# Performance work log

Hardware: AMD Instinct MI355X
Metric: run time of the kernel (lower is better)

## Reference

```python
import jax, jax.numpy as jnp
import numpy as np

A, D, H, NACT = 8, 128, 64, 16  # n_agents, input_shape, rnn_hidden_dim, n_actions
B = 16384


def setup_inputs() -> dict:
    key = jax.random.key(0)
    ks = jax.random.split(key, 12)
    s = 1.0 / np.sqrt(H)
    si = 1.0 / np.sqrt(D)
    inp = {
        'inputs': jax.random.normal(ks[0], (B * A, D), dtype=jnp.float32),
        'hidden_state': jax.random.normal(ks[1], (B, A, H), dtype=jnp.float32),
        # stacked per-agent (non-shared) weights, PyTorch default-init scale
        'W1': jax.random.uniform(ks[2], (A, H, D), jnp.float32, -si, si),
        'b1': jax.random.uniform(ks[3], (A, H), jnp.float32, -si, si),
        'W_ih': jax.random.uniform(ks[4], (A, 3 * H, H), jnp.float32, -s, s),
        'b_ih': jax.random.uniform(ks[5], (A, 3 * H), jnp.float32, -s, s),
        'W_hh': jax.random.uniform(ks[6], (A, 3 * H, H), jnp.float32, -s, s),
        'b_hh': jax.random.uniform(ks[7], (A, 3 * H), jnp.float32, -s, s),
        'W2': jax.random.uniform(ks[8], (A, NACT, H), jnp.float32, -s, s),
        'b2': jax.random.uniform(ks[9], (A, NACT), jnp.float32, -s, s),
    }
    return inp


def reference(inputs, hidden_state, W1, b1, W_ih, b_ih, W_hh, b_hh, W2, b2):
    x = inputs.reshape(-1, A, D)                 # [B, A, D]
    h = hidden_state.reshape(-1, A, H)           # [B, A, H]
    # fc1 + ReLU, batched over agents
    z1 = jax.nn.relu(jnp.einsum('bad,ahd->bah', x, W1) + b1)
    # GRUCell (PyTorch convention: gates r, z, n)
    gi = jnp.einsum('bah,agh->bag', z1, W_ih) + b_ih   # [B, A, 3H]
    gh = jnp.einsum('bah,agh->bag', h, W_hh) + b_hh
    i_r, i_z, i_n = jnp.split(gi, 3, axis=-1)
    h_r, h_z, h_n = jnp.split(gh, 3, axis=-1)
    r = jax.nn.sigmoid(i_r + h_r)
    z = jax.nn.sigmoid(i_z + h_z)
    n = jnp.tanh(i_n + r * h_n)
    h_new = (1.0 - z) * n + z * h                # [B, A, H]
    # fc2
    q = jnp.einsum('bah,anh->ban', h_new, W2) + b2   # [B, A, NACT]
    # match torch: cat(qs, dim=-1).view(-1, n_actions) == reshape [B*A, NACT]
    return q.reshape(-1, NACT), h_new
```

## Files before the change

kernel.cpp:

```cpp
#include <hip/hip_runtime.h>
#include <hip/hip_bf16.h>
#include <cstddef>

#define NAGENT 8
#define DIN    128
#define HID    64
#define NACT   16

typedef __attribute__((ext_vector_type(8))) short bf16x8;
typedef __attribute__((ext_vector_type(4))) float f32x4;

__device__ __forceinline__ short f2bf(float f) {
    __hip_bfloat16 h = __float2bfloat16(f);
    union { __hip_bfloat16 h; short s; } u; u.h = h;
    return u.s;
}
__device__ __forceinline__ float sigmoid_f(float v) { return 1.0f / (1.0f + __expf(-v)); }
__device__ __forceinline__ float tanh_f(float v) {
    v = fminf(fmaxf(v, -15.0f), 15.0f);
    float e = __expf(2.0f * v);
    return (e - 1.0f) / (e + 1.0f);
}
__device__ __forceinline__ bf16x8 cvt8pair(float4 v0, float4 v1) {
    bf16x8 r;
    r[0] = f2bf(v0.x); r[1] = f2bf(v0.y); r[2] = f2bf(v0.z); r[3] = f2bf(v0.w);
    r[4] = f2bf(v1.x); r[5] = f2bf(v1.y); r[6] = f2bf(v1.z); r[7] = f2bf(v1.w);
    return r;
}
__device__ __forceinline__ void gload_lds16(const void* g, void* l) {
    __builtin_amdgcn_global_load_lds(
        (const __attribute__((address_space(1))) unsigned int*)g,
        (__attribute__((address_space(3))) unsigned int*)l, 16, 0, 0);
}

extern "C" __global__ void __launch_bounds__(256)
conv_weights_packed(const float* __restrict__ W1, const float* __restrict__ Wih,
                    const float* __restrict__ Whh, const float* __restrict__ W2,
                    short* __restrict__ ws)
{
    const int a = blockIdx.y;
    const int c = blockIdx.x * 256 + threadIdx.x;
    if (c >= 4224) return;
    const int lane = c & 63, lr = lane & 15, lk = lane >> 4;
    const float* src;
    if (c < 1024) {
        int n = c >> 8, k = (c >> 6) & 3;
        src = W1 + a * 8192 + (n * 16 + lr) * 128 + k * 32 + lk * 8;
    } else if (c < 2560) {
        int idx = (c - 1024) >> 6;
        int g = idx >> 3, n = (idx >> 1) & 3, kk = idx & 1;
        src = Wih + a * 12288 + (g * 64 + n * 16 + lr) * 64 + kk * 32 + lk * 8;
    } else if (c < 4096) {
        int idx = (c - 2560) >> 6;
        int g = idx >> 3, n = (idx >> 1) & 3, kk = idx & 1;
        src = Whh + a * 12288 + (g * 64 + n * 16 + lr) * 64 + kk * 32 + lk * 8;
    } else {
        int kk = (c - 4096) >> 6;
        src = W2 + a * 1024 + lr * 64 + kk * 32 + lk * 8;
    }
    float4 v0 = ((const float4*)src)[0];
    float4 v1 = ((const float4*)src)[1];
    bf16x8 o = cvt8pair(v0, v1);
    *(bf16x8*)(ws + (size_t)a * 33792 + (size_t)c * 8) = o;
}

extern "C" __global__ void __launch_bounds__(256, 4)
rnn_main(const float* __restrict__ x,
         const float* __restrict__ hin,
         const float* __restrict__ b1, const float* __restrict__ bih,
         const float* __restrict__ bhh, const float* __restrict__ b2,
         const short* __restrict__ wsp,
         float* __restrict__ qout,
         float* __restrict__ hout)
{
    const int bid  = blockIdx.x;
    const int a    = bid & 7;
    const int t    = threadIdx.x;
    const int wid  = t >> 6;
    const int lane = t & 63;
    const int lr   = lane & 15;
    const int lk   = lane >> 4;

    __shared__ short wbuf[6144];
    __shared__ short zs[4 * 1024];
    char* zb = (char*)(zs + wid * 1024);

    const short* wsA = wsp + (size_t)a * 33792;
    const int tile = (bid >> 3) * 4 + wid;
    const int arow = tile * 16 + lr;

    const float* xrow = x + ((size_t)arow * NAGENT + a) * DIN + lk * 8;
    const float* hrow = hin + ((size_t)arow * NAGENT + a) * HID + lk * 8;

    gload_lds16(wsA + (size_t)(wid * 2 + 0) * 512 + lane * 8, wbuf + (wid * 2 + 0) * 512);
    gload_lds16(wsA + (size_t)(wid * 2 + 1) * 512 + lane * 8, wbuf + (wid * 2 + 1) * 512);

    bf16x8 xf[4];
    #pragma unroll
    for (int k = 0; k < 4; ++k)
        xf[k] = cvt8pair(*(const float4*)(xrow + k * 32),
                         *(const float4*)(xrow + k * 32 + 4));
    bf16x8 hf0 = cvt8pair(*(const float4*)(hrow),      *(const float4*)(hrow + 4));
    bf16x8 hf1 = cvt8pair(*(const float4*)(hrow + 32), *(const float4*)(hrow + 36));

    f32x4 acc1[4];
    #pragma unroll
    for (int n = 0; n < 4; ++n) {
        float bv = b1[a * HID + n * 16 + lr];
        acc1[n] = (f32x4){bv, bv, bv, bv};
    }

    __syncthreads();

    #pragma unroll
    for (int k = 0; k < 4; ++k)
        #pragma unroll
        for (int n = 0; n < 2; ++n) {
            bf16x8 wb = *(const bf16x8*)(wbuf + ((n * 4 + k) * 64 + lane) * 8);
            acc1[n] = __builtin_amdgcn_mfma_f32_16x16x32_bf16(xf[k], wb, acc1[n], 0, 0, 0);
        }
    __syncthreads();

    gload_lds16(wsA + (size_t)(8 + wid * 2 + 0) * 512 + lane * 8, wbuf + (wid * 2 + 0) * 512);
    gload_lds16(wsA + (size_t)(8 + wid * 2 + 1) * 512 + lane * 8, wbuf + (wid * 2 + 1) * 512);
    __syncthreads();

    #pragma unroll
    for (int k = 0; k < 4; ++k)
        #pragma unroll
        for (int n = 2; n < 4; ++n) {
            bf16x8 wb = *(const bf16x8*)(wbuf + (((n * 4 + k) - 8) * 64 + lane) * 8);
            acc1[n] = __builtin_amdgcn_mfma_f32_16x16x32_bf16(xf[k], wb, acc1[n], 0, 0, 0);
        }
    #pragma unroll
    for (int n = 0; n < 4; ++n)
        #pragma unroll
        for (int j = 0; j < 4; ++j) {
            int row = lk * 4 + j, col = n * 16 + lr;
            *(short*)(zb + row * 128 + ((col * 2) ^ ((row & 7) << 4))) =
                f2bf(fmaxf(acc1[n][j], 0.0f));
        }

    bf16x8 za0 = *(const bf16x8*)(zb + lr * 128 + ((0 * 64 + lk * 16) ^ ((lr & 7) << 4)));
    bf16x8 za1 = *(const bf16x8*)(zb + lr * 128 + ((1 * 64 + lk * 16) ^ ((lr & 7) << 4)));

    #pragma unroll 1
    for (int n = 0; n < 4; ++n) {
        __syncthreads();
        #pragma unroll
        for (int si = 0; si < 3; ++si) {
            int s = wid + si * 4;
            int round = (s < 6) ? (16 + ((s >> 1) * 4 + n) * 2 + (s & 1))
                                : (40 + (((s - 6) >> 1) * 4 + n) * 2 + ((s - 6) & 1));
            gload_lds16(wsA + (size_t)round * 512 + lane * 8, wbuf + s * 512);
        }
        float hp[4];
        #pragma unroll
        for (int j = 0; j < 4; ++j)
            hp[j] = hin[((size_t)(tile * 16 + lk * 4 + j) * NAGENT + a) * HID + n * 16 + lr];
        float bhr = bhh[a * 192 +   0 + n * 16 + lr];
        float bhz = bhh[a * 192 +  64 + n * 16 + lr];
        float bhn = bhh[a * 192 + 128 + n * 16 + lr];
        float bir = bih[a * 192 +   0 + n * 16 + lr];
        float biz = bih[a * 192 +  64 + n * 16 + lr];
        float bin_ = bih[a * 192 + 128 + n * 16 + lr];
        __syncthreads();

        f32x4 aHr = (f32x4){bhr, bhr, bhr, bhr};
        f32x4 aHz = (f32x4){bhz, bhz, bhz, bhz};
        f32x4 aHn = (f32x4){bhn, bhn, bhn, bhn};
        f32x4 aIr = (f32x4){bir, bir, bir, bir};
        f32x4 aIz = (f32x4){biz, biz, biz, biz};
        f32x4 aIn = (f32x4){bin_, bin_, bin_, bin_};
        #pragma unroll
        for (int kk = 0; kk < 2; ++kk) {
            bf16x8 hfk = kk ? hf1 : hf0;
            bf16x8 zak = kk ? za1 : za0;
            bf16x8 wir = *(const bf16x8*)(wbuf + ((0 * 2 + kk) * 64 + lane) * 8);
            bf16x8 wiz = *(const bf16x8*)(wbuf + ((1 * 2 + kk) * 64 + lane) * 8);
            bf16x8 win = *(const bf16x8*)(wbuf + ((2 * 2 + kk) * 64 + lane) * 8);
            bf16x8 whr = *(const bf16x8*)(wbuf + ((6 + 0 * 2 + kk) * 64 + lane) * 8);
            bf16x8 whz = *(const bf16x8*)(wbuf + ((6 + 1 * 2 + kk) * 64 + lane) * 8);
            bf16x8 whn = *(const bf16x8*)(wbuf + ((6 + 2 * 2 + kk) * 64 + lane) * 8);
            aHr = __builtin_amdgcn_mfma_f32_16x16x32_bf16(hfk, whr, aHr, 0, 0, 0);
            aHz = __builtin_amdgcn_mfma_f32_16x16x32_bf16(hfk, whz, aHz, 0, 0, 0);
            aHn = __builtin_amdgcn_mfma_f32_16x16x32_bf16(hfk, whn, aHn, 0, 0, 0);
            aIr = __builtin_amdgcn_mfma_f32_16x16x32_bf16(zak, wir, aIr, 0, 0, 0);
            aIz = __builtin_amdgcn_mfma_f32_16x16x32_bf16(zak, wiz, aIz, 0, 0, 0);
            aIn = __builtin_amdgcn_mfma_f32_16x16x32_bf16(zak, win, aIn, 0, 0, 0);
        }

        #pragma unroll
        for (int j = 0; j < 4; ++j) {
            int row = lk * 4 + j, col = n * 16 + lr;
            float r  = sigmoid_f(aIr[j] + aHr[j]);
            float zv = sigmoid_f(aIz[j] + aHz[j]);
            float nn = tanh_f(aIn[j] + r * aHn[j]);
            float hv = (1.0f - zv) * nn + zv * hp[j];
            hout[((size_t)(tile * 16 + row) * NAGENT + a) * HID + col] = hv;
            *(short*)(zb + row * 128 + ((col * 2) ^ ((row & 7) << 4))) = f2bf(hv);
        }
    }

    {
        float bq = b2[a * NACT + lr];
        f32x4 q = (f32x4){bq, bq, bq, bq};
        bf16x8 ha0 = *(const bf16x8*)(zb + lr * 128 + ((0 * 64 + lk * 16) ^ ((lr & 7) << 4)));
        bf16x8 ha1 = *(const bf16x8*)(zb + lr * 128 + ((1 * 64 + lk * 16) ^ ((lr & 7) << 4)));
        bf16x8 w2f0 = *(const bf16x8*)(wsA + 32768 + (0 * 64 + lane) * 8);
        bf16x8 w2f1 = *(const bf16x8*)(wsA + 32768 + (1 * 64 + lane) * 8);
        q = __builtin_amdgcn_mfma_f32_16x16x32_bf16(ha0, w2f0, q, 0, 0, 0);
        q = __builtin_amdgcn_mfma_f32_16x16x32_bf16(ha1, w2f1, q, 0, 0, 0);
        #pragma unroll
        for (int j = 0; j < 4; ++j)
            qout[((size_t)(tile * 16 + lk * 4 + j) * NAGENT + a) * NACT + lr] = q[j];
    }
}

extern "C" void kernel_launch(void* const* d_in, const int* in_sizes, int n_in,
                              void* d_out, int out_size, void* d_ws, size_t ws_size,
                              hipStream_t stream)
{
    const float* x   = (const float*)d_in[0];
    const float* hin = (const float*)d_in[1];
    const float* W1  = (const float*)d_in[2];
    const float* b1  = (const float*)d_in[3];
    const float* Wih = (const float*)d_in[4];
    const float* bih = (const float*)d_in[5];
    const float* Whh = (const float*)d_in[6];
    const float* bhh = (const float*)d_in[7];
    const float* W2  = (const float*)d_in[8];
    const float* b2  = (const float*)d_in[9];

    const int B = in_sizes[0] / (NAGENT * DIN);

    float* qout = (float*)d_out;
    float* hout = (float*)d_out + (size_t)B * NAGENT * NACT;

    short* wsp = (short*)d_ws;

    conv_weights_packed<<<dim3(17, NAGENT), 256, 0, stream>>>(W1, Wih, Whh, W2, wsp);

    dim3 grid((B / 64) * NAGENT);
    rnn_main<<<grid, 256, 0, stream>>>(x, hin, b1, bih, bhh, b2, wsp, qout, hout);
}
```

Baseline: 48.71 us.

## Double-buffer weight staging in LDS to overlap loads with MFMA

```diff
diff --git a/kernel.cpp b/kernel.cpp
--- a/kernel.cpp
+++ b/kernel.cpp
@@ -81,20 +81,26 @@
     const int lr   = lane & 15;
     const int lk   = lane >> 4;
 
-    __shared__ short wbuf[6144];
+    __shared__ short wbuf[2 * 3072];
     __shared__ short zs[4 * 1024];
     char* zb = (char*)(zs + wid * 1024);
+    const char* wb0 = (const char*)wbuf;
+    const char* wb1 = (const char*)(wbuf + 3072);
 
     const short* wsA = wsp + (size_t)a * 33792;
     const int tile = (bid >> 3) * 4 + wid;
     const int arow = tile * 16 + lr;
 
+    #define STAGE6(dstbuf, REXPR)                                                   \
+        { int s = wid;  int rr = (REXPR);                                           \
+          gload_lds16(wsA + (size_t)rr * 512 + lane * 8, (dstbuf) + s * 512);       \
+          if (wid < 2) { s = wid + 4; rr = (REXPR);                                 \
+            gload_lds16(wsA + (size_t)rr * 512 + lane * 8, (dstbuf) + s * 512); } }
+
+    STAGE6(wbuf, s)
+
     const float* xrow = x + ((size_t)arow * NAGENT + a) * DIN + lk * 8;
     const float* hrow = hin + ((size_t)arow * NAGENT + a) * HID + lk * 8;
-
-    gload_lds16(wsA + (size_t)(wid * 2 + 0) * 512 + lane * 8, wbuf + (wid * 2 + 0) * 512);
-    gload_lds16(wsA + (size_t)(wid * 2 + 1) * 512 + lane * 8, wbuf + (wid * 2 + 1) * 512);
-
     bf16x8 xf[4];
     #pragma unroll
     for (int k = 0; k < 4; ++k)
@@ -102,104 +108,110 @@
                          *(const float4*)(xrow + k * 32 + 4));
     bf16x8 hf0 = cvt8pair(*(const float4*)(hrow),      *(const float4*)(hrow + 4));
     bf16x8 hf1 = cvt8pair(*(const float4*)(hrow + 32), *(const float4*)(hrow + 36));
+    float b1v[4];
+    #pragma unroll
+    for (int n = 0; n < 4; ++n) b1v[n] = b1[a * HID + n * 16 + lr];
 
     f32x4 acc1[4];
     #pragma unroll
-    for (int n = 0; n < 4; ++n) {
-        float bv = b1[a * HID + n * 16 + lr];
-        acc1[n] = (f32x4){bv, bv, bv, bv};
-    }
-
-    __syncthreads();
-
-    #pragma unroll
-    for (int k = 0; k < 4; ++k)
-        #pragma unroll
-        for (int n = 0; n < 2; ++n) {
-            bf16x8 wb = *(const bf16x8*)(wbuf + ((n * 4 + k) * 64 + lane) * 8);
-            acc1[n] = __builtin_amdgcn_mfma_f32_16x16x32_bf16(xf[k], wb, acc1[n], 0, 0, 0);
-        }
-    __syncthreads();
-
-    gload_lds16(wsA + (size_t)(8 + wid * 2 + 0) * 512 + lane * 8, wbuf + (wid * 2 + 0) * 512);
-    gload_lds16(wsA + (size_t)(8 + wid * 2 + 1) * 512 + lane * 8, wbuf + (wid * 2 + 1) * 512);
-    __syncthreads();
-
-    #pragma unroll
-    for (int k = 0; k < 4; ++k)
-        #pragma unroll
-        for (int n = 2; n < 4; ++n) {
-            bf16x8 wb = *(const bf16x8*)(wbuf + (((n * 4 + k) - 8) * 64 + lane) * 8);
-            acc1[n] = __builtin_amdgcn_mfma_f32_16x16x32_bf16(xf[k], wb, acc1[n], 0, 0, 0);
-        }
+    for (int n = 0; n < 4; ++n) acc1[n] = (f32x4){0.f, 0.f, 0.f, 0.f};
+
+    __syncthreads();
+
+    STAGE6(wbuf + 3072, 6 + s)
+    #pragma unroll
+    for (int s = 0; s < 6; ++s) {
+        bf16x8 w = *(const bf16x8*)(wb0 + s * 1024 + lane * 16);
+        acc1[s >> 2] = __builtin_amdgcn_mfma_f32_16x16x32_bf16(xf[s & 3], w, acc1[s >> 2], 0, 0, 0);
+    }
+    __syncthreads();
+
+    gload_lds16(wsA + (size_t)(12 + wid) * 512 + lane * 8, wbuf + wid * 512);
+    #pragma unroll
+    for (int s = 0; s < 6; ++s) {
+        int f = 6 + s;
+        bf16x8 w = *(const bf16x8*)(wb1 + s * 1024 + lane * 16);
+        acc1[f >> 2] = __builtin_amdgcn_mfma_f32_16x16x32_bf16(xf[f & 3], w, acc1[f >> 2], 0, 0, 0);
+    }
+    __syncthreads();
+
+    STAGE6(wbuf + 3072, 16 + 0 * 2 + (s >> 1) * 8 + (s & 1))
+    #pragma unroll
+    for (int s = 0; s < 4; ++s) {
+        bf16x8 w = *(const bf16x8*)(wb0 + s * 1024 + lane * 16);
+        acc1[3] = __builtin_amdgcn_mfma_f32_16x16x32_bf16(xf[s], w, acc1[3], 0, 0, 0);
+    }
     #pragma unroll
     for (int n = 0; n < 4; ++n)
         #pragma unroll
         for (int j = 0; j < 4; ++j) {
             int row = lk * 4 + j, col = n * 16 + lr;
             *(short*)(zb + row * 128 + ((col * 2) ^ ((row & 7) << 4))) =
-                f2bf(fmaxf(acc1[n][j], 0.0f));
-        }
+                f2bf(fmaxf(acc1[n][j] + b1v[n], 0.0f));
+        }
+    __syncthreads();
 
     bf16x8 za0 = *(const bf16x8*)(zb + lr * 128 + ((0 * 64 + lk * 16) ^ ((lr & 7) << 4)));
     bf16x8 za1 = *(const bf16x8*)(zb + lr * 128 + ((1 * 64 + lk * 16) ^ ((lr & 7) << 4)));
 
     #pragma unroll 1
     for (int n = 0; n < 4; ++n) {
-        __syncthreads();
-        #pragma unroll
-        for (int si = 0; si < 3; ++si) {
-            int s = wid + si * 4;
-            int round = (s < 6) ? (16 + ((s >> 1) * 4 + n) * 2 + (s & 1))
-                                : (40 + (((s - 6) >> 1) * 4 + n) * 2 + ((s - 6) & 1));
-            gload_lds16(wsA + (size_t)round * 512 + lane * 8, wbuf + s * 512);
-        }
+        STAGE6(wbuf, 40 + n * 2 + (s >> 1) * 8 + (s & 1))
         float hp[4];
         #pragma unroll
         for (int j = 0; j < 4; ++j)
             hp[j] = hin[((size_t)(tile * 16 + lk * 4 + j) * NAGENT + a) * HID + n * 16 + lr];
-        float bhr = bhh[a * 192 +   0 + n * 16 + lr];
-        float bhz = bhh[a * 192 +  64 + n * 16 + lr];
-        float bhn = bhh[a * 192 + 128 + n * 16 + lr];
-        float bir = bih[a * 192 +   0 + n * 16 + lr];
-        float biz = bih[a * 192 +  64 + n * 16 + lr];
+        float bsr  = bih[a * 192 +   0 + n * 16 + lr] + bhh[a * 192 +   0 + n * 16 + lr];
+        float bsz  = bih[a * 192 +  64 + n * 16 + lr] + bhh[a * 192 +  64 + n * 16 + lr];
         float bin_ = bih[a * 192 + 128 + n * 16 + lr];
+        float bhn_ = bhh[a * 192 + 128 + n * 16 + lr];
+
+        f32x4 aI0 = (f32x4){0.f,0.f,0.f,0.f}, aI1 = aI0, aI2 = aI0;
+        {
+            bf16x8 w0 = *(const bf16x8*)(wb1 + 0 * 1024 + lane * 16);
+            bf16x8 w1 = *(const bf16x8*)(wb1 + 1 * 1024 + lane * 16);
+            bf16x8 w2 = *(const bf16x8*)(wb1 + 2 * 1024 + lane * 16);
+            bf16x8 w3 = *(const bf16x8*)(wb1 + 3 * 1024 + lane * 16);
+            bf16x8 w4 = *(const bf16x8*)(wb1 + 4 * 1024 + lane * 16);
+            bf16x8 w5 = *(const bf16x8*)(wb1 + 5 * 1024 + lane * 16);
+            aI0 = __builtin_amdgcn_mfma_f32_16x16x32_bf16(za0, w0, aI0, 0, 0, 0);
+            aI0 = __builtin_amdgcn_mfma_f32_16x16x32_bf16(za1, w1, aI0, 0, 0, 0);
+            aI1 = __builtin_amdgcn_mfma_f32_16x16x32_bf16(za0, w2, aI1, 0, 0, 0);
+            aI1 = __builtin_amdgcn_mfma_f32_16x16x32_bf16(za1, w3, aI1, 0, 0, 0);
+            aI2 = __builtin_amdgcn_mfma_f32_16x16x32_bf16(za0, w4, aI2, 0, 0, 0);
+            aI2 = __builtin_amdgcn_mfma_f32_16x16x32_bf16(za1, w5, aI2, 0, 0, 0);
+        }
         __syncthreads();
 
-        f32x4 aHr = (f32x4){bhr, bhr, bhr, bhr};
-        f32x4 aHz = (f32x4){bhz, bhz, bhz, bhz};
-        f32x4 aHn = (f32x4){bhn, bhn, bhn, bhn};
-        f32x4 aIr = (f32x4){bir, bir, bir, bir};
-        f32x4 aIz = (f32x4){biz, biz, biz, biz};
-        f32x4 aIn = (f32x4){bin_, bin_, bin_, bin_};
-        #pragma unroll
-        for (int kk = 0; kk < 2; ++kk) {
-            bf16x8 hfk = kk ? hf1 : hf0;
-            bf16x8 zak = kk ? za1 : za0;
-            bf16x8 wir = *(const bf16x8*)(wbuf + ((0 * 2 + kk) * 64 + lane) * 8);
-            bf16x8 wiz = *(const bf16x8*)(wbuf + ((1 * 2 + kk) * 64 + lane) * 8);
-            bf16x8 win = *(const bf16x8*)(wbuf + ((2 * 2 + kk) * 64 + lane) * 8);
-            bf16x8 whr = *(const bf16x8*)(wbuf + ((6 + 0 * 2 + kk) * 64 + lane) * 8);
-            bf16x8 whz = *(const bf16x8*)(wbuf + ((6 + 1 * 2 + kk) * 64 + lane) * 8);
-            bf16x8 whn = *(const bf16x8*)(wbuf + ((6 + 2 * 2 + kk) * 64 + lane) * 8);
-            aHr = __builtin_amdgcn_mfma_f32_16x16x32_bf16(hfk, whr, aHr, 0, 0, 0);
-            aHz = __builtin_amdgcn_mfma_f32_16x16x32_bf16(hfk, whz, aHz, 0, 0, 0);
-            aHn = __builtin_amdgcn_mfma_f32_16x16x32_bf16(hfk, whn, aHn, 0, 0, 0);
-            aIr = __builtin_amdgcn_mfma_f32_16x16x32_bf16(zak, wir, aIr, 0, 0, 0);
-            aIz = __builtin_amdgcn_mfma_f32_16x16x32_bf16(zak, wiz, aIz, 0, 0, 0);
-            aIn = __builtin_amdgcn_mfma_f32_16x16x32_bf16(zak, win, aIn, 0, 0, 0);
-        }
-
+        if (n < 3) {
+            STAGE6(wbuf + 3072, 16 + (n + 1) * 2 + (s >> 1) * 8 + (s & 1))
+        }
+        f32x4 aH0 = (f32x4){0.f,0.f,0.f,0.f}, aH1 = aH0, aH2 = aH0;
+        {
+            bf16x8 w0 = *(const bf16x8*)(wb0 + 0 * 1024 + lane * 16);
+            bf16x8 w1 = *(const bf16x8*)(wb0 + 1 * 1024 + lane * 16);
+            bf16x8 w2 = *(const bf16x8*)(wb0 + 2 * 1024 + lane * 16);
+            bf16x8 w3 = *(const bf16x8*)(wb0 + 3 * 1024 + lane * 16);
+            bf16x8 w4 = *(const bf16x8*)(wb0 + 4 * 1024 + lane * 16);
+            bf16x8 w5 = *(const bf16x8*)(wb0 + 5 * 1024 + lane * 16);
+            aH0 = __builtin_amdgcn_mfma_f32_16x16x32_bf16(hf0, w0, aH0, 0, 0, 0);
+            aH0 = __builtin_amdgcn_mfma_f32_16x16x32_bf16(hf1, w1, aH0, 0, 0, 0);
+            aH1 = __builtin_amdgcn_mfma_f32_16x16x32_bf16(hf0, w2, aH1, 0, 0, 0);
+            aH1 = __builtin_amdgcn_mfma_f32_16x16x32_bf16(hf1, w3, aH1, 0, 0, 0);
+            aH2 = __builtin_amdgcn_mfma_f32_16x16x32_bf16(hf0, w4, aH2, 0, 0, 0);
+            aH2 = __builtin_amdgcn_mfma_f32_16x16x32_bf16(hf1, w5, aH2, 0, 0, 0);
+        }
         #pragma unroll
         for (int j = 0; j < 4; ++j) {
             int row = lk * 4 + j, col = n * 16 + lr;
-            float r  = sigmoid_f(aIr[j] + aHr[j]);
-            float zv = sigmoid_f(aIz[j] + aHz[j]);
-            float nn = tanh_f(aIn[j] + r * aHn[j]);
+            float r  = sigmoid_f(aI0[j] + aH0[j] + bsr);
+            float zv = sigmoid_f(aI1[j] + aH1[j] + bsz);
+            float nn = tanh_f((aI2[j] + bin_) + r * (aH2[j] + bhn_));
             float hv = (1.0f - zv) * nn + zv * hp[j];
             hout[((size_t)(tile * 16 + row) * NAGENT + a) * HID + col] = hv;
             *(short*)(zb + row * 128 + ((col * 2) ^ ((row & 7) << 4))) = f2bf(hv);
         }
+        if (n < 3) __syncthreads();
     }
 
     {
@@ -215,6 +227,7 @@
         for (int j = 0; j < 4; ++j)
             qout[((size_t)(tile * 16 + lk * 4 + j) * NAGENT + a) * NACT + lr] = q[j];
     }
+    #undef STAGE6
 }
 
 extern "C" void kernel_launch(void* const* d_in, const int* in_sizes, int n_in,
```

Result: no change. 48.09 us (median of 2 runs) (-1.3%).
